# Kernel optimization log

Measured on AMD Instinct MI355X. Metric: run time of the kernel, lower is better.

## Reference

```python
import jax, jax.numpy as jnp
import numpy as np

P, G = 8192, 4096
SH_DEG = 2            # active_sh_degree = max_sh_degree = 2 -> 9 SH coeffs
N_SH = (SH_DEG + 1) ** 2
C0 = 0.28209479177387814
C1 = 0.4886025119029199
C2 = (1.0925484305920792, -1.0925484305920792, 0.31539156525252005,
      -1.0925484305920792, 0.5462742152960396)
CMIN, CMAX = 0.0, 1.0  # config.rendering.coord_min/max


def setup_inputs() -> dict:
    key = jax.random.key(0)
    ks = jax.random.split(key, 7)
    position_rx = jax.random.uniform(ks[0], (P, 3), dtype=jnp.float32)  # in [cmin,cmax]
    mean = jax.random.uniform(ks[1], (G, 3), dtype=jnp.float32) * 2.0 - 1.0
    features_dc = jax.random.uniform(ks[2], (G, 1, 1), dtype=jnp.float32) * 0.2 - 0.1
    features_rest = jax.random.normal(ks[3], (G, 1, N_SH - 1), dtype=jnp.float32) * 0.05
    scaling = jnp.float32(np.log(0.3)) + 0.1 * jax.random.normal(ks[4], (G, 3), dtype=jnp.float32)
    rotation = jax.random.normal(ks[5], (G, 4), dtype=jnp.float32)
    opacity = jax.random.normal(ks[6], (G, 1), dtype=jnp.float32)
    return dict(position_rx=position_rx, mean=mean, features_dc=features_dc,
                features_rest=features_rest, scaling=scaling, rotation=rotation,
                opacity=opacity)


def _quat_to_rot(q):
    # q: [G,4] (w,x,y,z), normalized (rotation_activation = F.normalize)
    q = q / jnp.linalg.norm(q, axis=-1, keepdims=True)
    r, x, y, z = q[:, 0], q[:, 1], q[:, 2], q[:, 3]
    R = jnp.stack([
        jnp.stack([1 - 2 * (y * y + z * z), 2 * (x * y - r * z), 2 * (x * z + r * y)], -1),
        jnp.stack([2 * (x * y + r * z), 1 - 2 * (x * x + z * z), 2 * (y * z - r * x)], -1),
        jnp.stack([2 * (x * z - r * y), 2 * (y * z + r * x), 1 - 2 * (x * x + y * y)], -1),
    ], axis=-2)  # [G,3,3]
    return R


def _eval_sh(sh, dirs):
    # sh: [G, 9]; dirs: [P, G, 3] unit vectors -> [P, G]
    x, y, z = dirs[..., 0], dirs[..., 1], dirs[..., 2]
    res = C0 * sh[:, 0]
    res = (res - C1 * y * sh[:, 1] + C1 * z * sh[:, 2] - C1 * x * sh[:, 3])
    xx, yy, zz = x * x, y * y, z * z
    res = (res
           + C2[0] * (x * y) * sh[:, 4]
           + C2[1] * (y * z) * sh[:, 5]
           + C2[2] * (2.0 * zz - xx - yy) * sh[:, 6]
           + C2[3] * (x * z) * sh[:, 7]
           + C2[4] * (xx - yy) * sh[:, 8])
    return res


def reference(position_rx, mean, features_dc, features_rest, scaling, rotation, opacity):
    # normalize_points: map [cmin,cmax] -> [-1,1]
    q = (position_rx - CMIN) / (CMAX - CMIN) * 2.0 - 1.0  # [P,3]

    # covariance_activation: Sigma = L L^T, L = R diag(s); use precision directly
    scales = jnp.exp(scaling)                    # [G,3]
    inv_var = 1.0 / (scales * scales)            # [G,3]
    R = _quat_to_rot(rotation)                   # [G,3,3]
    Sinv = jnp.einsum('gik,gk,gjk->gij', R, inv_var, R)  # Sigma^{-1} [G,3,3]

    diff = q[:, None, :] - mean[None, :, :]      # [P,G,3]
    mahal = jnp.einsum('pgi,gij,pgj->pg', diff, Sinv, diff)  # [P,G]
    gauss = jnp.exp(-0.5 * mahal)                # [P,G]

    # eval_features: normalized direction point -> gaussian, SH evaluation
    dirs = diff / (jnp.linalg.norm(diff, axis=-1, keepdims=True) + 1e-8)
    sh = jnp.concatenate([features_dc, features_rest], axis=-1)[:, 0, :]  # [G,9]
    feat = _eval_sh(sh, dirs)                    # [P,G]

    alpha = jax.nn.sigmoid(opacity)[:, 0]        # [G]
    out = jnp.einsum('pg,g->p', feat * gauss, alpha)  # splat accumulate
    return out[:, None]                          # [P,1]
```

## Files before the change

kernel.cpp:

```cpp
#include <hip/hip_runtime.h>
#include <hip/hip_bf16.h>

constexpr int P = 8192;
constexpr int G = 4096;
constexpr int BLK = 256;
constexpr int GSPLIT = 128;
constexpr int CHUNK = G / GSPLIT;
constexpr int PPT = 8;
constexpr int NH = PPT / 2;
constexpr int PBLK = BLK * PPT;
constexpr float LOG2E = 1.4426950408889634f;

typedef float v2f __attribute__((ext_vector_type(2)));

__device__ __forceinline__ float fast_exp2(float x) {
  float r;
  asm("v_exp_f32 %0, %1" : "=v"(r) : "v"(x));
  return r;
}

__global__ __launch_bounds__(BLK) void fused_main(
    const float* __restrict__ pos,
    const float* __restrict__ mean, const float* __restrict__ fdc,
    const float* __restrict__ frest, const float* __restrict__ scal,
    const float* __restrict__ rot, const float* __restrict__ opac,
    float* __restrict__ partial) {
  __shared__ float4 sg[CHUNK * 5];

  const int t = threadIdx.x;
  const int c = blockIdx.y;
  const int pbase = blockIdx.x * PBLK + t;

  v2f pxv[NH], pyv[NH], pzv[NH], accv[NH];
#pragma unroll
  for (int h = 0; h < NH; ++h) {
    const int pA = pbase + (2 * h + 0) * BLK;
    const int pB = pbase + (2 * h + 1) * BLK;
    v2f x = {pos[pA * 3 + 0], pos[pB * 3 + 0]};
    v2f y = {pos[pA * 3 + 1], pos[pB * 3 + 1]};
    v2f z = {pos[pA * 3 + 2], pos[pB * 3 + 2]};
    pxv[h] = x * 2.0f - 1.0f;
    pyv[h] = y * 2.0f - 1.0f;
    pzv[h] = z * 2.0f - 1.0f;
    accv[h] = (v2f){0.f, 0.f};
  }

  if (t < CHUNK) {
    const int g = c * CHUNK + t;

    float qr = rot[g * 4 + 0], qx = rot[g * 4 + 1];
    float qy = rot[g * 4 + 2], qz = rot[g * 4 + 3];
    float qn = 1.0f / sqrtf(qr * qr + qx * qx + qy * qy + qz * qz);
    qr *= qn; qx *= qn; qy *= qn; qz *= qn;

    float R00 = 1.f - 2.f * (qy * qy + qz * qz);
    float R01 = 2.f * (qx * qy - qr * qz);
    float R02 = 2.f * (qx * qz + qr * qy);
    float R10 = 2.f * (qx * qy + qr * qz);
    float R11 = 1.f - 2.f * (qx * qx + qz * qz);
    float R12 = 2.f * (qy * qz - qr * qx);
    float R20 = 2.f * (qx * qz - qr * qy);
    float R21 = 2.f * (qy * qz + qr * qx);
    float R22 = 1.f - 2.f * (qx * qx + qy * qy);

    float sc0 = expf(scal[g * 3 + 0]);
    float sc1 = expf(scal[g * 3 + 1]);
    float sc2 = expf(scal[g * 3 + 2]);
    float iv0 = 1.0f / (sc0 * sc0);
    float iv1 = 1.0f / (sc1 * sc1);
    float iv2 = 1.0f / (sc2 * sc2);

    float s00 = R00 * R00 * iv0 + R01 * R01 * iv1 + R02 * R02 * iv2;
    float s11 = R10 * R10 * iv0 + R11 * R11 * iv1 + R12 * R12 * iv2;
    float s22 = R20 * R20 * iv0 + R21 * R21 * iv1 + R22 * R22 * iv2;
    float s01 = R00 * R10 * iv0 + R01 * R11 * iv1 + R02 * R12 * iv2;
    float s02 = R00 * R20 * iv0 + R01 * R21 * iv1 + R02 * R22 * iv2;
    float s12 = R10 * R20 * iv0 + R11 * R21 * iv1 + R12 * R22 * iv2;

    const float kD = -0.5f * LOG2E;
    const float kO = -LOG2E;

    float alpha = 1.0f / (1.0f + expf(-opac[g]));

    const float C0 = 0.28209479177387814f;
    const float C1 = 0.4886025119029199f;
    float a0 = C0 * fdc[g] * alpha;
    float a1 = -C1 * frest[g * 8 + 0] * alpha;
    float a2 =  C1 * frest[g * 8 + 1] * alpha;
    float a3 = -C1 * frest[g * 8 + 2] * alpha;
    float a4 =  1.0925484305920792f  * frest[g * 8 + 3] * alpha;
    float a5 = -1.0925484305920792f  * frest[g * 8 + 4] * alpha;
    float a6 =  0.31539156525252005f * frest[g * 8 + 5] * alpha;
    float a7 = -1.0925484305920792f  * frest[g * 8 + 6] * alpha;
    float a8 =  0.5462742152960396f  * frest[g * 8 + 7] * alpha;

    float mx = mean[g * 3 + 0], my = mean[g * 3 + 1], mz = mean[g * 3 + 2];

    sg[t * 5 + 0] = make_float4(mx, my, mz, kD * s00);
    sg[t * 5 + 1] = make_float4(kD * s11, kD * s22, kO * s01, kO * s02);
    sg[t * 5 + 2] = make_float4(kO * s12, a0, a1, a2);
    sg[t * 5 + 3] = make_float4(a3, a4, a5, a7);
    sg[t * 5 + 4] = make_float4(a8 - a6, -a8 - a6, 2.f * a6, 0.f);
  }

  __syncthreads();

#pragma unroll 2
  for (int gi = 0; gi < CHUNK; ++gi) {
    const float4 v0 = sg[gi * 5 + 0];
    const float4 v1 = sg[gi * 5 + 1];
    const float4 v2 = sg[gi * 5 + 2];
    const float4 v3 = sg[gi * 5 + 3];
    const float4 v4 = sg[gi * 5 + 4];

#pragma unroll
    for (int h = 0; h < NH; ++h) {
      const v2f dx = pxv[h] - v0.x;
      const v2f dy = pyv[h] - v0.y;
      const v2f dz = pzv[h] - v0.z;
      const v2f dxx = dx * dx, dyy = dy * dy, dzz = dz * dz;
      const v2f dxdy = dx * dy, dxdz = dx * dz, dydz = dy * dz;
      const v2f d2 = dxx + dyy + dzz;

      v2f m = v0.w * dxx;
      m = v1.x * dyy + m;
      m = v1.y * dzz + m;
      m = v1.z * dxdy + m;
      m = v1.w * dxdz + m;
      m = v2.x * dydz + m;
      v2f gauss;
      gauss.x = fast_exp2(m.x);
      gauss.y = fast_exp2(m.y);

      const v2f d2c = __builtin_elementwise_max(d2, (v2f){1e-16f, 1e-16f});
      v2f inv;
      inv.x = __builtin_amdgcn_rsqf(d2c.x);
      inv.y = __builtin_amdgcn_rsqf(d2c.y);
      const v2f inv2 = inv * inv;

      v2f lin = v2.z * dy;
      lin = v2.w * dz + lin;
      lin = v3.x * dx + lin;

      v2f quad = v3.y * dxdy;
      quad = v3.z * dydz + quad;
      quad = v3.w * dxdz + quad;
      quad = v4.x * dxx + quad;
      quad = v4.y * dyy + quad;
      quad = v4.z * dzz + quad;

      v2f feat = inv * lin + v2.y;
      feat = inv2 * quad + feat;

      accv[h] = gauss * feat + accv[h];
    }
  }

#pragma unroll
  for (int h = 0; h < NH; ++h) {
    partial[(size_t)c * P + pbase + (2 * h + 0) * BLK] = accv[h].x;
    partial[(size_t)c * P + pbase + (2 * h + 1) * BLK] = accv[h].y;
  }
}

__global__ __launch_bounds__(256) void reduce_kernel(
    const float* __restrict__ partial, float* __restrict__ out) {
  __shared__ float red[4][64];
  const int t = threadIdx.x;
  const int lane = t & 63;
  const int s = t >> 6;
  const int p = blockIdx.x * 64 + lane;
  const int cbase = s * 32;

  float a0 = 0.f, a1 = 0.f, a2 = 0.f, a3 = 0.f;
#pragma unroll
  for (int j = 0; j < 32; j += 4) {
    a0 += partial[(size_t)(cbase + j + 0) * P + p];
    a1 += partial[(size_t)(cbase + j + 1) * P + p];
    a2 += partial[(size_t)(cbase + j + 2) * P + p];
    a3 += partial[(size_t)(cbase + j + 3) * P + p];
  }
  red[s][lane] = (a0 + a1) + (a2 + a3);
  __syncthreads();

  if (t < 64) {
    out[p] = (red[0][lane] + red[1][lane]) + (red[2][lane] + red[3][lane]);
  }
}

extern "C" void kernel_launch(void* const* d_in, const int* in_sizes, int n_in,
                              void* d_out, int out_size, void* d_ws, size_t ws_size,
                              hipStream_t stream) {
  const float* pos   = (const float*)d_in[0];
  const float* mean  = (const float*)d_in[1];
  const float* fdc   = (const float*)d_in[2];
  const float* frest = (const float*)d_in[3];
  const float* scal  = (const float*)d_in[4];
  const float* rot   = (const float*)d_in[5];
  const float* opac  = (const float*)d_in[6];
  float* out = (float*)d_out;

  float* partial = (float*)d_ws;

  fused_main<<<dim3(P / PBLK, GSPLIT), BLK, 0, stream>>>(
      pos, mean, fdc, frest, scal, rot, opac, partial);
  reduce_kernel<<<P / 64, 256, 0, stream>>>(partial, out);
}
```

Measured before the change: 30.81 us.

## Split per-Gaussian precompute into its own kernel and stream params via scalar loads

Moves the per-Gaussian covariance and SH coefficient setup into a separate precompute kernel that writes packed float4 records to workspace. The main kernel then reads those records through inline-asm s_load_dwordx4 scalar loads, double-buffered, instead of shared memory plus __syncthreads. It also halves points per thread, which doubles the grid. The aim is to drop the redundant per-block setup, the LDS traffic and the barrier, at the cost of an extra kernel launch and hand-written waitcnt scheduling. The last iteration also issues a prefetch one record past the chunk, which reads into the next chunk or past the end of the precompute buffer.

```diff
diff --git a/kernel.cpp b/kernel.cpp
--- a/kernel.cpp
+++ b/kernel.cpp
@@ -6,12 +6,13 @@
 constexpr int BLK = 256;
 constexpr int GSPLIT = 128;
 constexpr int CHUNK = G / GSPLIT;
-constexpr int PPT = 8;
+constexpr int PPT = 4;
 constexpr int NH = PPT / 2;
 constexpr int PBLK = BLK * PPT;
 constexpr float LOG2E = 1.4426950408889634f;
 
 typedef float v2f __attribute__((ext_vector_type(2)));
+typedef float sf4 __attribute__((ext_vector_type(4)));
 
 __device__ __forceinline__ float fast_exp2(float x) {
   float r;
@@ -19,17 +20,90 @@
   return r;
 }
 
-__global__ __launch_bounds__(BLK) void fused_main(
-    const float* __restrict__ pos,
+__global__ __launch_bounds__(256) void precomp_kernel(
     const float* __restrict__ mean, const float* __restrict__ fdc,
     const float* __restrict__ frest, const float* __restrict__ scal,
     const float* __restrict__ rot, const float* __restrict__ opac,
+    float4* __restrict__ pre) {
+  int g = blockIdx.x * blockDim.x + threadIdx.x;
+  if (g >= G) return;
+
+  float qr = rot[g * 4 + 0], qx = rot[g * 4 + 1];
+  float qy = rot[g * 4 + 2], qz = rot[g * 4 + 3];
+  float qn = 1.0f / sqrtf(qr * qr + qx * qx + qy * qy + qz * qz);
+  qr *= qn; qx *= qn; qy *= qn; qz *= qn;
+
+  float R00 = 1.f - 2.f * (qy * qy + qz * qz);
+  float R01 = 2.f * (qx * qy - qr * qz);
+  float R02 = 2.f * (qx * qz + qr * qy);
+  float R10 = 2.f * (qx * qy + qr * qz);
+  float R11 = 1.f - 2.f * (qx * qx + qz * qz);
+  float R12 = 2.f * (qy * qz - qr * qx);
+  float R20 = 2.f * (qx * qz - qr * qy);
+  float R21 = 2.f * (qy * qz + qr * qx);
+  float R22 = 1.f - 2.f * (qx * qx + qy * qy);
+
+  float sc0 = expf(scal[g * 3 + 0]);
+  float sc1 = expf(scal[g * 3 + 1]);
+  float sc2 = expf(scal[g * 3 + 2]);
+  float iv0 = 1.0f / (sc0 * sc0);
+  float iv1 = 1.0f / (sc1 * sc1);
+  float iv2 = 1.0f / (sc2 * sc2);
+
+  float s00 = R00 * R00 * iv0 + R01 * R01 * iv1 + R02 * R02 * iv2;
+  float s11 = R10 * R10 * iv0 + R11 * R11 * iv1 + R12 * R12 * iv2;
+  float s22 = R20 * R20 * iv0 + R21 * R21 * iv1 + R22 * R22 * iv2;
+  float s01 = R00 * R10 * iv0 + R01 * R11 * iv1 + R02 * R12 * iv2;
+  float s02 = R00 * R20 * iv0 + R01 * R21 * iv1 + R02 * R22 * iv2;
+  float s12 = R10 * R20 * iv0 + R11 * R21 * iv1 + R12 * R22 * iv2;
+
+  const float kD = -0.5f * LOG2E;
+  const float kO = -LOG2E;
+
+  float alpha = 1.0f / (1.0f + expf(-opac[g]));
+
+  const float C0 = 0.28209479177387814f;
+  const float C1 = 0.4886025119029199f;
+  float a0 = C0 * fdc[g] * alpha;
+  float a1 = -C1 * frest[g * 8 + 0] * alpha;
+  float a2 =  C1 * frest[g * 8 + 1] * alpha;
+  float a3 = -C1 * frest[g * 8 + 2] * alpha;
+  float a4 =  1.0925484305920792f  * frest[g * 8 + 3] * alpha;
+  float a5 = -1.0925484305920792f  * frest[g * 8 + 4] * alpha;
+  float a6 =  0.31539156525252005f * frest[g * 8 + 5] * alpha;
+  float a7 = -1.0925484305920792f  * frest[g * 8 + 6] * alpha;
+  float a8 =  0.5462742152960396f  * frest[g * 8 + 7] * alpha;
+
+  float mx = mean[g * 3 + 0], my = mean[g * 3 + 1], mz = mean[g * 3 + 2];
+
+  pre[g * 5 + 0] = make_float4(mx, my, mz, kD * s00);
+  pre[g * 5 + 1] = make_float4(kD * s11, kD * s22, kO * s01, kO * s02);
+  pre[g * 5 + 2] = make_float4(kO * s12, a0, a1, a2);
+  pre[g * 5 + 3] = make_float4(a3, a4, a5, a7);
+  pre[g * 5 + 4] = make_float4(a8 - a6, -a8 - a6, 2.f * a6, 0.f);
+}
+
+#define SLOAD(b0, b1, b2, b3, b4, addr)                 \
+  asm volatile("s_load_dwordx4 %0, %5, 0x0\n\t"         \
+               "s_load_dwordx4 %1, %5, 0x10\n\t"        \
+               "s_load_dwordx4 %2, %5, 0x20\n\t"        \
+               "s_load_dwordx4 %3, %5, 0x30\n\t"        \
+               "s_load_dwordx4 %4, %5, 0x40"            \
+               : "=&s"(b0), "=&s"(b1), "=&s"(b2), "=&s"(b3), "=&s"(b4) \
+               : "s"(addr))
+
+#define SWAIT(b0, b1, b2, b3, b4)                       \
+  asm volatile("s_waitcnt lgkmcnt(0)"                   \
+               : "+s"(b0), "+s"(b1), "+s"(b2), "+s"(b3), "+s"(b4))
+
+__global__ __launch_bounds__(BLK) void main_kernel(
+    const float* __restrict__ pos, const float* __restrict__ pre,
     float* __restrict__ partial) {
-  __shared__ float4 sg[CHUNK * 5];
-
   const int t = threadIdx.x;
   const int c = blockIdx.y;
   const int pbase = blockIdx.x * PBLK + t;
+
+  const float* gbase = pre + (size_t)c * CHUNK * 20;
 
   v2f pxv[NH], pyv[NH], pzv[NH], accv[NH];
 #pragma unroll
@@ -45,89 +119,22 @@
     accv[h] = (v2f){0.f, 0.f};
   }
 
-  if (t < CHUNK) {
-    const int g = c * CHUNK + t;
-
-    float qr = rot[g * 4 + 0], qx = rot[g * 4 + 1];
-    float qy = rot[g * 4 + 2], qz = rot[g * 4 + 3];
-    float qn = 1.0f / sqrtf(qr * qr + qx * qx + qy * qy + qz * qz);
-    qr *= qn; qx *= qn; qy *= qn; qz *= qn;
-
-    float R00 = 1.f - 2.f * (qy * qy + qz * qz);
-    float R01 = 2.f * (qx * qy - qr * qz);
-    float R02 = 2.f * (qx * qz + qr * qy);
-    float R10 = 2.f * (qx * qy + qr * qz);
-    float R11 = 1.f - 2.f * (qx * qx + qz * qz);
-    float R12 = 2.f * (qy * qz - qr * qx);
-    float R20 = 2.f * (qx * qz - qr * qy);
-    float R21 = 2.f * (qy * qz + qr * qx);
-    float R22 = 1.f - 2.f * (qx * qx + qy * qy);
-
-    float sc0 = expf(scal[g * 3 + 0]);
-    float sc1 = expf(scal[g * 3 + 1]);
-    float sc2 = expf(scal[g * 3 + 2]);
-    float iv0 = 1.0f / (sc0 * sc0);
-    float iv1 = 1.0f / (sc1 * sc1);
-    float iv2 = 1.0f / (sc2 * sc2);
-
-    float s00 = R00 * R00 * iv0 + R01 * R01 * iv1 + R02 * R02 * iv2;
-    float s11 = R10 * R10 * iv0 + R11 * R11 * iv1 + R12 * R12 * iv2;
-    float s22 = R20 * R20 * iv0 + R21 * R21 * iv1 + R22 * R22 * iv2;
-    float s01 = R00 * R10 * iv0 + R01 * R11 * iv1 + R02 * R12 * iv2;
-    float s02 = R00 * R20 * iv0 + R01 * R21 * iv1 + R02 * R22 * iv2;
-    float s12 = R10 * R20 * iv0 + R11 * R21 * iv1 + R12 * R22 * iv2;
-
-    const float kD = -0.5f * LOG2E;
-    const float kO = -LOG2E;
-
-    float alpha = 1.0f / (1.0f + expf(-opac[g]));
-
-    const float C0 = 0.28209479177387814f;
-    const float C1 = 0.4886025119029199f;
-    float a0 = C0 * fdc[g] * alpha;
-    float a1 = -C1 * frest[g * 8 + 0] * alpha;
-    float a2 =  C1 * frest[g * 8 + 1] * alpha;
-    float a3 = -C1 * frest[g * 8 + 2] * alpha;
-    float a4 =  1.0925484305920792f  * frest[g * 8 + 3] * alpha;
-    float a5 = -1.0925484305920792f  * frest[g * 8 + 4] * alpha;
-    float a6 =  0.31539156525252005f * frest[g * 8 + 5] * alpha;
-    float a7 = -1.0925484305920792f  * frest[g * 8 + 6] * alpha;
-    float a8 =  0.5462742152960396f  * frest[g * 8 + 7] * alpha;
-
-    float mx = mean[g * 3 + 0], my = mean[g * 3 + 1], mz = mean[g * 3 + 2];
-
-    sg[t * 5 + 0] = make_float4(mx, my, mz, kD * s00);
-    sg[t * 5 + 1] = make_float4(kD * s11, kD * s22, kO * s01, kO * s02);
-    sg[t * 5 + 2] = make_float4(kO * s12, a0, a1, a2);
-    sg[t * 5 + 3] = make_float4(a3, a4, a5, a7);
-    sg[t * 5 + 4] = make_float4(a8 - a6, -a8 - a6, 2.f * a6, 0.f);
-  }
-
-  __syncthreads();
-
-#pragma unroll 2
-  for (int gi = 0; gi < CHUNK; ++gi) {
-    const float4 v0 = sg[gi * 5 + 0];
-    const float4 v1 = sg[gi * 5 + 1];
-    const float4 v2 = sg[gi * 5 + 2];
-    const float4 v3 = sg[gi * 5 + 3];
-    const float4 v4 = sg[gi * 5 + 4];
-
+  auto compute = [&](sf4 c0, sf4 c1, sf4 c2, sf4 c3, sf4 c4) {
 #pragma unroll
     for (int h = 0; h < NH; ++h) {
-      const v2f dx = pxv[h] - v0.x;
-      const v2f dy = pyv[h] - v0.y;
-      const v2f dz = pzv[h] - v0.z;
+      const v2f dx = pxv[h] - c0.x;
+      const v2f dy = pyv[h] - c0.y;
+      const v2f dz = pzv[h] - c0.z;
       const v2f dxx = dx * dx, dyy = dy * dy, dzz = dz * dz;
       const v2f dxdy = dx * dy, dxdz = dx * dz, dydz = dy * dz;
       const v2f d2 = dxx + dyy + dzz;
 
-      v2f m = v0.w * dxx;
-      m = v1.x * dyy + m;
-      m = v1.y * dzz + m;
-      m = v1.z * dxdy + m;
-      m = v1.w * dxdz + m;
-      m = v2.x * dydz + m;
+      v2f m = c0.w * dxx;
+      m = c1.x * dyy + m;
+      m = c1.y * dzz + m;
+      m = c1.z * dxdy + m;
+      m = c1.w * dxdz + m;
+      m = c2.x * dydz + m;
       v2f gauss;
       gauss.x = fast_exp2(m.x);
       gauss.y = fast_exp2(m.y);
@@ -138,23 +145,37 @@
       inv.y = __builtin_amdgcn_rsqf(d2c.y);
       const v2f inv2 = inv * inv;
 
-      v2f lin = v2.z * dy;
-      lin = v2.w * dz + lin;
-      lin = v3.x * dx + lin;
-
-      v2f quad = v3.y * dxdy;
-      quad = v3.z * dydz + quad;
-      quad = v3.w * dxdz + quad;
-      quad = v4.x * dxx + quad;
-      quad = v4.y * dyy + quad;
-      quad = v4.z * dzz + quad;
-
-      v2f feat = inv * lin + v2.y;
+      v2f lin = c2.z * dy;
+      lin = c2.w * dz + lin;
+      lin = c3.x * dx + lin;
+
+      v2f quad = c3.y * dxdy;
+      quad = c3.z * dydz + quad;
+      quad = c3.w * dxdz + quad;
+      quad = c4.x * dxx + quad;
+      quad = c4.y * dyy + quad;
+      quad = c4.z * dzz + quad;
+
+      v2f feat = inv * lin + c2.y;
       feat = inv2 * quad + feat;
 
       accv[h] = gauss * feat + accv[h];
     }
-  }
+  };
+
+  sf4 A0, A1, A2, A3, A4, B0, B1, B2, B3, B4;
+
+  SLOAD(A0, A1, A2, A3, A4, gbase);
+#pragma unroll 2
+  for (int gi = 0; gi < CHUNK; gi += 2) {
+    SWAIT(A0, A1, A2, A3, A4);
+    SLOAD(B0, B1, B2, B3, B4, gbase + (gi + 1) * 20);
+    compute(A0, A1, A2, A3, A4);
+    SWAIT(B0, B1, B2, B3, B4);
+    SLOAD(A0, A1, A2, A3, A4, gbase + (gi + 2) * 20);
+    compute(B0, B1, B2, B3, B4);
+  }
+  asm volatile("s_waitcnt lgkmcnt(0)");
 
 #pragma unroll
   for (int h = 0; h < NH; ++h) {
@@ -200,9 +221,10 @@
   const float* opac  = (const float*)d_in[6];
   float* out = (float*)d_out;
 
-  float* partial = (float*)d_ws;
-
-  fused_main<<<dim3(P / PBLK, GSPLIT), BLK, 0, stream>>>(
-      pos, mean, fdc, frest, scal, rot, opac, partial);
+  float4* pre = (float4*)d_ws;
+  float* partial = (float*)((char*)d_ws + (size_t)G * 5 * sizeof(float4));
+
+  precomp_kernel<<<G / 256, 256, 0, stream>>>(mean, fdc, frest, scal, rot, opac, pre);
+  main_kernel<<<dim3(P / PBLK, GSPLIT), BLK, 0, stream>>>(pos, (const float*)pre, partial);
   reduce_kernel<<<P / 64, 256, 0, stream>>>(partial, out);
 }
```

Result: slower. 38.13 us (+23.7%).
